# Kernel optimization log

Hardware: AMD Instinct MI355X
Metric: run time of the kernel (lower is better)

## Reference

```python
import jax, jax.numpy as jnp
import numpy as np

E = 256
H = 512
LN_EPS = 1e-5
NORM_EPS = 1e-12


def setup_inputs() -> dict:
    key = jax.random.key(0)
    ks = jax.random.split(key, 8)
    B, N, M = 8, 128, 128
    track_features = jax.random.normal(ks[0], (B, N, E), dtype=jnp.float32)
    det_features = jax.random.normal(ks[1], (B, M, E), dtype=jnp.float32)
    # MLP params (torch Linear default init style: uniform, but values irrelevant for correctness harness)
    lim1 = 1.0 / np.sqrt(3 * E)
    W1 = jax.random.uniform(ks[2], (3 * E, H), minval=-lim1, maxval=lim1, dtype=jnp.float32)
    b1 = jax.random.uniform(ks[3], (H,), minval=-lim1, maxval=lim1, dtype=jnp.float32)
    gamma = jnp.ones((H,), dtype=jnp.float32)
    beta = jnp.zeros((H,), dtype=jnp.float32)
    lim2 = 1.0 / np.sqrt(H)
    W2 = jax.random.uniform(ks[4], (H, 1), minval=-lim2, maxval=lim2, dtype=jnp.float32)
    b2 = jax.random.uniform(ks[5], (1,), minval=-lim2, maxval=lim2, dtype=jnp.float32)
    return {"track_features": track_features, "det_features": det_features,
            "W1": W1, "b1": b1, "gamma": gamma, "beta": beta, "W2": W2, "b2": b2}


def _l2_normalize(x):
    # F.normalize(x, dim=-1): x / max(||x||_2, eps)
    n = jnp.sqrt(jnp.sum(x * x, axis=-1, keepdims=True))
    return x / jnp.maximum(n, NORM_EPS)


def reference(track_features, det_features, W1, b1, gamma, beta, W2, b2):
    t = _l2_normalize(track_features)   # (B, N, E)
    d = _l2_normalize(det_features)     # (B, M, E)
    tb = t[:, :, None, :]               # (B, N, 1, E)
    db = d[:, None, :, :]               # (B, 1, M, E)
    B, N, _ = t.shape
    M = d.shape[1]
    diff = jnp.abs(tb - db)                                  # (B, N, M, E)
    pair = jnp.concatenate([jnp.broadcast_to(tb, (B, N, M, E)),
                            jnp.broadcast_to(db, (B, N, M, E)),
                            diff], axis=-1)                  # (B, N, M, 3E)
    h = jnp.einsum('bnme,eh->bnmh', pair, W1) + b1           # (B, N, M, H)
    mu = jnp.mean(h, axis=-1, keepdims=True)
    var = jnp.mean((h - mu) ** 2, axis=-1, keepdims=True)
    h = (h - mu) * jax.lax.rsqrt(var + LN_EPS) * gamma + beta
    h = h * jax.nn.sigmoid(h)                                # SiLU
    out = jnp.einsum('bnmh,ho->bnmo', h, W2)[..., 0] + b2[0]  # (B, N, M)
    return out
```

## Files before the change

kernel.cpp:

```cpp
#include <hip/hip_runtime.h>
#include <hip/hip_bf16.h>
#include <cstdint>

typedef __bf16 bf16x8 __attribute__((ext_vector_type(8)));
typedef __bf16 bf16x2 __attribute__((ext_vector_type(2)));
typedef float f32x4 __attribute__((ext_vector_type(4)));

#define E_DIM 256
#define H_DIM 512

static __device__ __forceinline__ unsigned pkbf(float a, float b) {
    bf16x2 h;
    h[0] = (__bf16)a;
    h[1] = (__bf16)b;
    return __builtin_bit_cast(unsigned, h);
}

__global__ __launch_bounds__(512, 2)
void prep_kernel(const float* __restrict__ track, const float* __restrict__ det,
                 const float* __restrict__ W1, const float* __restrict__ b1,
                 float* __restrict__ P, float* __restrict__ Q,
                 __bf16* __restrict__ W1cc, float* __restrict__ sclT,
                 float* __restrict__ sclD) {
    __shared__ __align__(16) __bf16 Ash[16 * 256];
    int tid = threadIdx.x;
    int blk = blockIdx.x;

    if (blk >= 256) {
        int u = (blk - 256) * 512 + tid;
        int j = u & 3;
        int h = (u >> 2) & 511;
        int c = u >> 11;
        const float* src = W1 + (size_t)(512 + c * 32 + j * 8) * H_DIM + h;
        uint4 v;
        v.x = pkbf(src[0],                 src[(size_t)1 * H_DIM]);
        v.y = pkbf(src[(size_t)2 * H_DIM], src[(size_t)3 * H_DIM]);
        v.z = pkbf(src[(size_t)4 * H_DIM], src[(size_t)5 * H_DIM]);
        v.w = pkbf(src[(size_t)6 * H_DIM], src[(size_t)7 * H_DIM]);
        *(uint4*)(W1cc + ((size_t)(c * 512 + h) * 32 + j * 8)) = v;
        return;
    }

    int lane = tid & 63;
    int wave = tid >> 6;
    int lq   = lane >> 4;
    int lc   = lane & 15;
    int l5   = lane & 31;

    int mat  = blk >> 7;
    int rowg = (blk >> 1) & 63;
    int half = blk & 1;
    int r0   = rowg * 16;
    int h0   = half * 256;
    const float* src = mat ? det : track;

    {
        int row = wave * 2 + (lane >> 5);
        const float* gp = src + (size_t)(r0 + row) * E_DIM + l5 * 8;
        float4 x0 = *(const float4*)gp;
        float4 x1 = *(const float4*)(gp + 4);
        float ss = x0.x*x0.x + x0.y*x0.y + x0.z*x0.z + x0.w*x0.w
                 + x1.x*x1.x + x1.y*x1.y + x1.z*x1.z + x1.w*x1.w;
#pragma unroll
        for (int off = 16; off > 0; off >>= 1) ss += __shfl_xor(ss, off);
        float st = 1.0f / fmaxf(sqrtf(ss), 1e-12f);
        if (half == 0 && l5 == 0) (mat ? sclD : sclT)[r0 + row] = st;
        uint4 v;
        v.x = pkbf(x0.x * st, x0.y * st);
        v.y = pkbf(x0.z * st, x0.w * st);
        v.z = pkbf(x1.x * st, x1.y * st);
        v.w = pkbf(x1.z * st, x1.w * st);
        int cc = l5 >> 2, j = l5 & 3;
        *(uint4*)&Ash[(size_t)(cc * 64 + j * 16 + row) * 8] = v;
    }
    __syncthreads();

    int hB = h0 + wave * 32 + lc;
    const float* wb = W1 + (size_t)(mat * 256) * H_DIM + hB;
    float wf[2][8];
#pragma unroll
    for (int ht = 0; ht < 2; ++ht)
#pragma unroll
        for (int i = 0; i < 8; ++i)
            wf[ht][i] = wb[(size_t)(lq * 8 + i) * H_DIM + ht * 16];

    f32x4 acc[2];
    acc[0] = (f32x4){0.f, 0.f, 0.f, 0.f};
    acc[1] = (f32x4){0.f, 0.f, 0.f, 0.f};

#pragma unroll
    for (int c = 0; c < 8; ++c) {
        bf16x8 cw[2];
#pragma unroll
        for (int ht = 0; ht < 2; ++ht) {
            uint4 u;
            u.x = pkbf(wf[ht][0], wf[ht][1]);
            u.y = pkbf(wf[ht][2], wf[ht][3]);
            u.z = pkbf(wf[ht][4], wf[ht][5]);
            u.w = pkbf(wf[ht][6], wf[ht][7]);
            cw[ht] = __builtin_bit_cast(bf16x8, u);
        }
        if (c < 7) {
            const float* nb = wb + (size_t)((c + 1) * 32 + lq * 8) * H_DIM;
#pragma unroll
            for (int ht = 0; ht < 2; ++ht)
#pragma unroll
                for (int i = 0; i < 8; ++i)
                    wf[ht][i] = nb[(size_t)i * H_DIM + ht * 16];
        }
        bf16x8 af = *(const bf16x8*)&Ash[(size_t)(c * 64 + lane) * 8];
#pragma unroll
        for (int ht = 0; ht < 2; ++ht)
            acc[ht] = __builtin_amdgcn_mfma_f32_16x16x32_bf16(cw[ht], af, acc[ht], 0, 0, 0);
    }

    float* dst = mat ? Q : P;
#pragma unroll
    for (int ht = 0; ht < 2; ++ht) {
        int h = h0 + wave * 32 + ht * 16 + lq * 4;
        f32x4 o = acc[ht];
        if (!mat) o += *(const f32x4*)&b1[h];
        *(f32x4*)&dst[(size_t)(r0 + lc) * H_DIM + h] = o;
    }
}

__global__ __launch_bounds__(512, 4)
void main_kernel(const float* __restrict__ track, const float* __restrict__ det,
                 const __bf16* __restrict__ W1cc,
                 const float* __restrict__ P, const float* __restrict__ Q,
                 const float* __restrict__ sclT, const float* __restrict__ sclD,
                 const float* __restrict__ gamma, const float* __restrict__ beta,
                 const float* __restrict__ W2, const float* __restrict__ b2,
                 float* __restrict__ out) {
    __shared__ __align__(16) char SMEM[46336];
    __bf16* Ash  = (__bf16*)SMEM;
    float*  LNr1 = (float*)(SMEM + 32768);
    float*  LNr2 = (float*)(SMEM + 35072);
    float*  Red2 = (float*)(SMEM + 37376);
    float*  MuS  = (float*)(SMEM + 39680);
    float*  RsS  = (float*)(SMEM + 39936);
    float*  Gs   = (float*)(SMEM + 40192);
    float*  Bs   = (float*)(SMEM + 42240);
    float*  Ws   = (float*)(SMEM + 44288);

    int tid  = threadIdx.x;
    int lane = tid & 63;
    int wave = tid >> 6;
    int lq   = lane >> 4;
    int lc   = lane & 15;

    int blk = blockIdx.x;
    int b   = blk >> 8;
    int n0  = ((blk >> 4) & 15) * 8;
    int m0  = (blk & 15) * 8;
    int gn  = b * 128 + n0;
    int gm  = b * 128 + m0;

    float b2v = b2[0];
    Gs[tid] = gamma[tid];
    Bs[tid] = beta[tid];
    Ws[tid] = W2[tid];

    const uint4* Wg = (const uint4*)W1cc;
    int hb = wave * 64 + lc;
    bf16x8 bwA[4], bwB[4];
#pragma unroll
    for (int ht = 0; ht < 4; ++ht)
        bwA[ht] = __builtin_bit_cast(bf16x8, Wg[(hb + ht * 16) * 4 + lq]);

    int k0 = wave * 32 + lq * 8;
    int ml = lane & 7;
    float sd = sclD[gm + ml];
    const float* dr = det + (size_t)(gm + ml) * E_DIM + k0;
    float4 d0 = *(const float4*)dr;
    float4 d1 = *(const float4*)(dr + 4);
#pragma unroll
    for (int r = 0; r < 4; ++r) {
        int nl = r * 2 + (lc >> 3);
        float st = sclT[gn + nl];
        const float* tr = track + (size_t)(gn + nl) * E_DIM + k0;
        float4 t0 = *(const float4*)tr;
        float4 t1 = *(const float4*)(tr + 4);
        uint4 v;
        v.x = pkbf(fabsf(t0.x * st - d0.x * sd), fabsf(t0.y * st - d0.y * sd));
        v.y = pkbf(fabsf(t0.z * st - d0.z * sd), fabsf(t0.w * st - d0.w * sd));
        v.z = pkbf(fabsf(t1.x * st - d1.x * sd), fabsf(t1.y * st - d1.y * sd));
        v.w = pkbf(fabsf(t1.z * st - d1.z * sd), fabsf(t1.w * st - d1.w * sd));
        *(uint4*)&Ash[(size_t)(r * 512 + wave * 64 + lane) * 8] = v;
    }

    const float* Pb = P + (size_t)gn * H_DIM;
    const float* Qb = Q + (size_t)gm * H_DIM;
    f32x4 acc[4][4];
    {
        f32x4 qv[4];
#pragma unroll
        for (int ht = 0; ht < 4; ++ht)
            qv[ht] = *(const f32x4*)&Qb[(size_t)ml * H_DIM + wave * 64 + ht * 16 + lq * 4];
#pragma unroll
        for (int pt = 0; pt < 4; ++pt) {
            int n = pt * 2 + (lc >> 3);
#pragma unroll
            for (int ht = 0; ht < 4; ++ht) {
                f32x4 pv = *(const f32x4*)&Pb[(size_t)n * H_DIM + wave * 64 + ht * 16 + lq * 4];
                acc[pt][ht] = pv + qv[ht];
            }
        }
    }
    __syncthreads();

#pragma unroll 2
    for (int c = 0; c < 8; ++c) {
        bf16x8* cur = (c & 1) ? bwB : bwA;
        bf16x8* nxt = (c & 1) ? bwA : bwB;
        int c1 = (c + 1) & 7;
#pragma unroll
        for (int ht = 0; ht < 4; ++ht)
            nxt[ht] = __builtin_bit_cast(bf16x8, Wg[c1 * 2048 + (hb + ht * 16) * 4 + lq]);
#pragma unroll
        for (int pt = 0; pt < 4; ++pt) {
            bf16x8 af = *(const bf16x8*)&Ash[(size_t)((pt * 8 + c) * 64 + lane) * 8];
#pragma unroll
            for (int ht = 0; ht < 4; ++ht)
                acc[pt][ht] = __builtin_amdgcn_mfma_f32_16x16x32_bf16(cur[ht], af, acc[pt][ht], 0, 0, 0);
        }
    }

#pragma unroll
    for (int pt = 0; pt < 4; ++pt) {
        float s1 = 0.f, s2 = 0.f;
#pragma unroll
        for (int ht = 0; ht < 4; ++ht)
#pragma unroll
            for (int rg = 0; rg < 4; ++rg) {
                float v = acc[pt][ht][rg];
                s1 += v; s2 += v * v;
            }
        s1 += __shfl_xor(s1, 16); s2 += __shfl_xor(s2, 16);
        s1 += __shfl_xor(s1, 32); s2 += __shfl_xor(s2, 32);
        if (lq == 0) {
            LNr1[(pt * 16 + lc) * 9 + wave] = s1;
            LNr2[(pt * 16 + lc) * 9 + wave] = s2;
        }
    }
    __syncthreads();
    {
        int p = tid >> 3, w = tid & 7;
        float s1 = LNr1[p * 9 + w];
        float s2 = LNr2[p * 9 + w];
        s1 += __shfl_xor(s1, 1); s2 += __shfl_xor(s2, 1);
        s1 += __shfl_xor(s1, 2); s2 += __shfl_xor(s2, 2);
        s1 += __shfl_xor(s1, 4); s2 += __shfl_xor(s2, 4);
        if (w == 0) {
            float mu  = s1 * (1.0f / 512.0f);
            float var = s2 * (1.0f / 512.0f) - mu * mu;
            MuS[p] = mu;
            RsS[p] = rsqrtf(var + 1e-5f);
        }
    }
    __syncthreads();

    float mus[4], rss[4];
#pragma unroll
    for (int pt = 0; pt < 4; ++pt) { mus[pt] = MuS[pt * 16 + lc]; rss[pt] = RsS[pt * 16 + lc]; }
    float ca[4] = {0.f, 0.f, 0.f, 0.f};
#pragma unroll
    for (int ht = 0; ht < 4; ++ht) {
        int h = wave * 64 + ht * 16 + lq * 4;
        f32x4 g  = *(const f32x4*)&Gs[h];
        f32x4 bb = *(const f32x4*)&Bs[h];
        f32x4 w  = *(const f32x4*)&Ws[h];
#pragma unroll
        for (int pt = 0; pt < 4; ++pt) {
#pragma unroll
            for (int rg = 0; rg < 4; ++rg) {
                float x = (acc[pt][ht][rg] - mus[pt]) * rss[pt] * g[rg] + bb[rg];
                float sg = __builtin_amdgcn_rcpf(1.0f + __expf(-x));
                ca[pt] += x * sg * w[rg];
            }
        }
    }
#pragma unroll
    for (int pt = 0; pt < 4; ++pt) {
        float cg = ca[pt];
        cg += __shfl_xor(cg, 16);
        cg += __shfl_xor(cg, 32);
        if (lq == 0) Red2[(pt * 16 + lc) * 9 + wave] = cg;
    }
    __syncthreads();
    {
        int p = tid >> 3, w = tid & 7;
        float cg = Red2[p * 9 + w];
        cg += __shfl_xor(cg, 1);
        cg += __shfl_xor(cg, 2);
        cg += __shfl_xor(cg, 4);
        if (w == 0)
            out[(size_t)(gn + (p >> 3)) * 128 + m0 + (p & 7)] = b2v + cg;
    }
}

extern "C" void kernel_launch(void* const* d_in, const int* in_sizes, int n_in,
                              void* d_out, int out_size, void* d_ws, size_t ws_size,
                              hipStream_t stream) {
    const float* track = (const float*)d_in[0];
    const float* det   = (const float*)d_in[1];
    const float* W1    = (const float*)d_in[2];
    const float* b1    = (const float*)d_in[3];
    const float* gamma = (const float*)d_in[4];
    const float* beta  = (const float*)d_in[5];
    const float* W2    = (const float*)d_in[6];
    const float* b2    = (const float*)d_in[7];
    float* out = (float*)d_out;

    char* ws = (char*)d_ws;
    float*  Pp   = (float*)(ws);
    float*  Qp   = (float*)(ws + (2u << 20));
    __bf16* W1cc = (__bf16*)(ws + (4u << 20));
    float*  sclT = (float*)(ws + (4u << 20) + (256u << 10));
    float*  sclD = (float*)(ws + (4u << 20) + (264u << 10));

    prep_kernel<<<288, 512, 0, stream>>>(track, det, W1, b1, Pp, Qp, W1cc, sclT, sclD);
    main_kernel<<<2048, 512, 0, stream>>>(track, det, W1cc, Pp, Qp, sclT, sclD,
                                          gamma, beta, W2, b2, out);
}
```

Before: 143.5 us.

## Remap blocks across XCDs for locality and pack LayerNorm/SiLU math into float2

```diff
diff --git a/kernel.cpp b/kernel.cpp
--- a/kernel.cpp
+++ b/kernel.cpp
@@ -5,6 +5,7 @@
 typedef __bf16 bf16x8 __attribute__((ext_vector_type(8)));
 typedef __bf16 bf16x2 __attribute__((ext_vector_type(2)));
 typedef float f32x4 __attribute__((ext_vector_type(4)));
+typedef float f32x2 __attribute__((ext_vector_type(2)));
 
 #define E_DIM 256
 #define H_DIM 512
@@ -149,10 +150,12 @@
     int lq   = lane >> 4;
     int lc   = lane & 15;
 
-    int blk = blockIdx.x;
-    int b   = blk >> 8;
-    int n0  = ((blk >> 4) & 15) * 8;
-    int m0  = (blk & 15) * 8;
+    int i   = blockIdx.x;
+    int xcd = i & 7;
+    int t8  = (i >> 3) & 31;
+    int b   = i >> 8;
+    int n0  = ((xcd >> 1) * 4 + (t8 >> 3)) * 8;
+    int m0  = ((xcd & 1) * 8 + (t8 & 7)) * 8;
     int gn  = b * 128 + n0;
     int gm  = b * 128 + m0;
 
@@ -228,14 +231,18 @@
 
 #pragma unroll
     for (int pt = 0; pt < 4; ++pt) {
-        float s1 = 0.f, s2 = 0.f;
-#pragma unroll
-        for (int ht = 0; ht < 4; ++ht)
-#pragma unroll
-            for (int rg = 0; rg < 4; ++rg) {
-                float v = acc[pt][ht][rg];
-                s1 += v; s2 += v * v;
+        f32x2 s1v = (f32x2){0.f, 0.f}, s2v = (f32x2){0.f, 0.f};
+#pragma unroll
+        for (int ht = 0; ht < 4; ++ht) {
+#pragma unroll
+            for (int hf = 0; hf < 2; ++hf) {
+                f32x2 v = (f32x2){acc[pt][ht][hf * 2], acc[pt][ht][hf * 2 + 1]};
+                s1v += v;
+                s2v += v * v;
             }
+        }
+        float s1 = s1v[0] + s1v[1];
+        float s2 = s2v[0] + s2v[1];
         s1 += __shfl_xor(s1, 16); s2 += __shfl_xor(s2, 16);
         s1 += __shfl_xor(s1, 32); s2 += __shfl_xor(s2, 32);
         if (lq == 0) {
@@ -263,7 +270,9 @@
     float mus[4], rss[4];
 #pragma unroll
     for (int pt = 0; pt < 4; ++pt) { mus[pt] = MuS[pt * 16 + lc]; rss[pt] = RsS[pt * 16 + lc]; }
-    float ca[4] = {0.f, 0.f, 0.f, 0.f};
+    f32x2 cav[4];
+#pragma unroll
+    for (int pt = 0; pt < 4; ++pt) cav[pt] = (f32x2){0.f, 0.f};
 #pragma unroll
     for (int ht = 0; ht < 4; ++ht) {
         int h = wave * 64 + ht * 16 + lq * 4;
@@ -272,17 +281,27 @@
         f32x4 w  = *(const f32x4*)&Ws[h];
 #pragma unroll
         for (int pt = 0; pt < 4; ++pt) {
-#pragma unroll
-            for (int rg = 0; rg < 4; ++rg) {
-                float x = (acc[pt][ht][rg] - mus[pt]) * rss[pt] * g[rg] + bb[rg];
-                float sg = __builtin_amdgcn_rcpf(1.0f + __expf(-x));
-                ca[pt] += x * sg * w[rg];
+            f32x2 mu2 = (f32x2){mus[pt], mus[pt]};
+            f32x2 rs2 = (f32x2){rss[pt], rss[pt]};
+#pragma unroll
+            for (int hf = 0; hf < 2; ++hf) {
+                f32x2 v  = (f32x2){acc[pt][ht][hf * 2], acc[pt][ht][hf * 2 + 1]};
+                f32x2 gg = (f32x2){g[hf * 2],  g[hf * 2 + 1]};
+                f32x2 bv = (f32x2){bb[hf * 2], bb[hf * 2 + 1]};
+                f32x2 wv = (f32x2){w[hf * 2],  w[hf * 2 + 1]};
+                f32x2 x  = (v - mu2) * rs2 * gg + bv;
+                f32x2 e, sg;
+                e[0]  = __expf(-x[0]);
+                e[1]  = __expf(-x[1]);
+                sg[0] = __builtin_amdgcn_rcpf(1.0f + e[0]);
+                sg[1] = __builtin_amdgcn_rcpf(1.0f + e[1]);
+                cav[pt] += x * sg * wv;
             }
         }
     }
 #pragma unroll
     for (int pt = 0; pt < 4; ++pt) {
-        float cg = ca[pt];
+        float cg = cav[pt][0] + cav[pt][1];
         cg += __shfl_xor(cg, 16);
         cg += __shfl_xor(cg, 32);
         if (lq == 0) Red2[(pt * 16 + lc) * 9 + wave] = cg;
```

Result: no change. 143.2 us (-0.2%).
